# Optimization experiments

Hardware: AMD Instinct MI355X
Metric: run time of the kernel (lower is better)

Reference implementation:

```python
import jax, jax.numpy as jnp
import numpy as np

N = 2000
E = 20000
C = 16
B = 128
N_IN = 200   # first N_IN nodes are input nodes
N_OUT = 200  # last N_OUT nodes are output nodes
EPS = 1e-5


def setup_inputs() -> dict:
    key = jax.random.key(0)
    ks = jax.random.split(key, 8)
    x = jax.random.normal(ks[0], (B, N), dtype=jnp.float32)
    edge_index = jax.random.randint(ks[1], (2, E), 0, N, dtype=jnp.int32)
    input_node_mask = jnp.arange(N) < N_IN
    output_node_mask = jnp.arange(N) >= (N - N_OUT)
    func_mask = ~(input_node_mask | output_node_mask)
    # sparse-linear parameters (structured forms of W1/W2/W3)
    w1 = jax.random.normal(ks[2], (E, C), dtype=jnp.float32) * (1.0 / np.sqrt(C))
    b1 = jnp.zeros((N, C), dtype=jnp.float32)
    w2 = jax.random.normal(ks[3], (N, C, C), dtype=jnp.float32) * (1.0 / np.sqrt(C))
    b2 = jnp.zeros((N, C), dtype=jnp.float32)
    w3 = jax.random.normal(ks[4], (E, C), dtype=jnp.float32) * 1.0  # d=1 init scale
    b3 = jnp.zeros((E,), dtype=jnp.float32)
    g1 = jnp.ones((N * C,), dtype=jnp.float32)
    be1 = jnp.zeros((N * C,), dtype=jnp.float32)
    g2 = jnp.ones((N * C,), dtype=jnp.float32)
    be2 = jnp.zeros((N * C,), dtype=jnp.float32)
    return {"x": x, "w1": w1, "b1": b1, "w2": w2, "b2": b2, "w3": w3, "b3": b3,
            "g1": g1, "be1": be1, "g2": g2, "be2": be2,
            "edge_index": edge_index, "func_mask": func_mask,
            "output_node_mask": output_node_mask, "layers": 4}


def _batchnorm(h, g, b):
    # training-mode BatchNorm1d: batch mean and biased variance over axis 0
    m = h.mean(axis=0)
    v = h.var(axis=0)
    return (h - m) * jax.lax.rsqrt(v + EPS) * g + b


def reference(x, w1, b1, w2, b2, w3, b3, g1, be1, g2, be2,
              edge_index, func_mask, output_node_mask, layers):
    src, dst = edge_index[0], edge_index[1]
    Bsz, Nn = x.shape
    Ee, Cc = w1.shape
    fm = func_mask.astype(x.dtype)
    w2m = w2 * fm[:, None, None]          # W2 blocks exist only at function nodes
    w3m = w3 * fm[src][:, None]           # W3 rows exist only for edges with src in function nodes

    x0 = x[:, src]                        # node2edge: (B, E)
    xe = x0
    for _ in range(layers):
        # lin1: scatter edge values into dst node hidden channels
        contrib = xe.T[:, :, None] * w1[:, None, :]                    # (E, B, C)
        h = jax.ops.segment_sum(contrib, dst, num_segments=Nn)         # (N, B, C)
        h = jnp.transpose(h, (1, 0, 2)) + b1                           # (B, N, C)
        h = _batchnorm(h.reshape(Bsz, Nn * Cc), g1, be1)
        h = jax.nn.elu(h).reshape(Bsz, Nn, Cc)
        # lin2: block-diagonal C x C mix per (function) node
        h = jnp.einsum('bnc,ncd->bnd', h, w2m) + b2
        h = _batchnorm(h.reshape(Bsz, Nn * Cc), g2, be2)
        h = jax.nn.elu(h).reshape(Bsz, Nn, Cc)
        # lin3: gather src hidden, per-edge dot back to edge space
        xe = jnp.einsum('bec,ec->be', h[:, src], w3m) + b3             # (B, E)
        xe = xe + x0
    # edge2node: scatter-sum edge values to dst nodes, keep output nodes
    nodes = jax.ops.segment_sum(xe.T, dst, num_segments=Nn)            # (N, B)
    return nodes.T * output_node_mask.astype(x.dtype)
```

## Files before the change

### kernel.cpp

```cpp
#include <hip/hip_runtime.h>
#include <math.h>

#define BB 128
#define NN 2000
#define EE 20000
#define CC 16
#define FUNC_LO 200
#define FUNC_HI 1800
#define OUT_LO 1800
#define NFUNC 1600
#define EPSV 1e-5f
#define SS 40
#define HP 129

__global__ __launch_bounds__(256) void k_prep(
    const float* __restrict__ x, const int* __restrict__ ei,
    const float* __restrict__ w1, const float* __restrict__ w3,
    const float* __restrict__ b3,
    int* __restrict__ degIn, int* __restrict__ degOut,
    int* __restrict__ posIn,
    float* __restrict__ xT, float* __restrict__ w1s, float* __restrict__ w3s,
    float* __restrict__ b3s, int* __restrict__ inoff, int* __restrict__ wout,
    int* __restrict__ dstn, float* __restrict__ out)
{
    int t = blockIdx.x * 256 + threadIdx.x;
    if (t < EE) {
        int s = ei[t], d = ei[EE + t];
        int p = atomicAdd(&degIn[d], 1);
        int q = atomicAdd(&degOut[s], 1);
        int pi = d * SS + p, po = s * SS + q;
        posIn[t] = pi;
        inoff[pi] = s * BB;
        wout[po]  = pi * BB;
        dstn[po]  = d;
        b3s[po]   = b3[t];
        const float4* w1r = (const float4*)(w1 + (size_t)t * CC);
        float4*       w1d = (float4*)(w1s + (size_t)pi * CC);
        const float4* w3r = (const float4*)(w3 + (size_t)t * CC);
        float4*       w3d = (float4*)(w3s + (size_t)po * CC);
        #pragma unroll
        for (int i = 0; i < 4; i++) { w1d[i] = w1r[i]; w3d[i] = w3r[i]; }
    }
    if (t < NN * BB) {
        int b = t / NN, n = t - b * NN;
        xT[n * BB + b] = x[t];
        out[t] = 0.0f;
    }
}

__global__ __launch_bounds__(128) void k_fill(
    const int* __restrict__ ei, const int* __restrict__ posIn,
    const float* __restrict__ b3, const float* __restrict__ xT,
    float* __restrict__ xeA, float* __restrict__ xeB, float* __restrict__ out)
{
    int e = blockIdx.x;
    int s = ei[e];
    if (s >= FUNC_LO && s < FUNC_HI) return;
    int d = ei[EE + e];
    int b = threadIdx.x;
    float val = b3[e] + xT[s * BB + b];
    if (d >= FUNC_LO && d < FUNC_HI) {
        int ro = posIn[e] * BB;
        xeA[ro + b] = val;
        xeB[ro + b] = val;
    } else if (d >= OUT_LO) {
        atomicAdd(&out[(size_t)b * NN + d], val);
    }
}

__device__ __forceinline__ void bn_elu(float (&t)[CC],
                                       const float* __restrict__ g,
                                       const float* __restrict__ be,
                                       float* tile, float* part_s, float* part_ss,
                                       float* sc, float* sh, int b) {
    #pragma unroll
    for (int c = 0; c < CC; c++) tile[c * HP + b] = t[c];
    __syncthreads();
    {
        int c = b & 15, grp = b >> 4;
        float s = 0.f, ss = 0.f;
        #pragma unroll
        for (int i = 0; i < 16; i++) {
            float v = tile[c * HP + grp * 16 + i];
            s += v; ss += v * v;
        }
        part_s[grp * 16 + c] = s;
        part_ss[grp * 16 + c] = ss;
    }
    __syncthreads();
    if (b < CC) {
        float S = 0.f, SSm = 0.f;
        #pragma unroll
        for (int g8 = 0; g8 < 8; g8++) { S += part_s[g8 * 16 + b]; SSm += part_ss[g8 * 16 + b]; }
        float mean = S * (1.0f / BB);
        float var = SSm * (1.0f / BB) - mean * mean;
        float scale = rsqrtf(var + EPSV) * g[b];
        sc[b] = scale;
        sh[b] = be[b] - mean * scale;
    }
    __syncthreads();
    #pragma unroll
    for (int c = 0; c < CC; c++) {
        float u = t[c] * sc[c] + sh[c];
        t[c] = (u > 0.0f) ? u : (__expf(u) - 1.0f);
    }
}

__global__ __launch_bounds__(128) void k_layer(
    const float* __restrict__ xe_in, const int* __restrict__ inoff,
    const float* __restrict__ xT,
    const float* __restrict__ w1s, const float* __restrict__ w2,
    const float* __restrict__ w3s, const float* __restrict__ b3s,
    const int* __restrict__ wout, const int* __restrict__ dstn,
    const float* __restrict__ g1, const float* __restrict__ be1,
    const float* __restrict__ g2, const float* __restrict__ be2,
    const int* __restrict__ degIn, const int* __restrict__ degOut,
    float* __restrict__ xe_out, float* __restrict__ out, int lastFlag)
{
    const int b = threadIdx.x;
    const int n = FUNC_LO + blockIdx.x;
    const int base = n * SS;

    __shared__ float tile[CC * HP];
    __shared__ float part_s[128], part_ss[128];
    __shared__ float sc[CC], sh[CC];

    int dIn = degIn[n];
    int dOut = degOut[n];
    float x0r = xT[n * BB + b];

    float a[CC];
    #pragma unroll
    for (int c = 0; c < CC; c++) a[c] = 0.0f;

    for (int k0 = 0; k0 < dIn; k0 += 8) {
        float v[8];
        #pragma unroll
        for (int j = 0; j < 8; j++) {
            v[j] = 0.0f;
            if (k0 + j < dIn) {
                int ro = inoff ? inoff[base + k0 + j] : (base + k0 + j) * BB;
                v[j] = xe_in[ro + b];
            }
        }
        #pragma unroll
        for (int j = 0; j < 8; j++) {
            if (k0 + j < dIn) {
                const float* wr = &w1s[(size_t)(base + k0 + j) * CC];
                #pragma unroll
                for (int c = 0; c < CC; c++) a[c] += v[j] * wr[c];
            }
        }
    }

    bn_elu(a, g1 + n * CC, be1 + n * CC, tile, part_s, part_ss, sc, sh, b);

    float h2[CC];
    #pragma unroll
    for (int d = 0; d < CC; d++) h2[d] = 0.0f;
    const float* w2n = w2 + n * (CC * CC);
    #pragma unroll
    for (int c = 0; c < CC; c++) {
        float av = a[c];
        #pragma unroll
        for (int d = 0; d < CC; d++) h2[d] += av * w2n[c * CC + d];
    }

    bn_elu(h2, g2 + n * CC, be2 + n * CC, tile, part_s, part_ss, sc, sh, b);

    for (int q0 = 0; q0 < dOut; q0 += 4) {
        #pragma unroll
        for (int j = 0; j < 4; j++) {
            int q = q0 + j;
            if (q >= dOut) break;
            int sl = base + q;
            int dn = dstn[sl];
            bool live = lastFlag ? (dn >= OUT_LO) : (dn >= FUNC_LO && dn < FUNC_HI);
            if (!live) continue;
            const float* wr = &w3s[(size_t)sl * CC];
            float val = b3s[sl] + x0r;
            #pragma unroll
            for (int d = 0; d < CC; d++) val += h2[d] * wr[d];
            if (lastFlag) atomicAdd(&out[(size_t)b * NN + dn], val);
            else          xe_out[wout[sl] + b] = val;
        }
    }
}

extern "C" void kernel_launch(void* const* d_in, const int* in_sizes, int n_in,
                              void* d_out, int out_size, void* d_ws, size_t ws_size,
                              hipStream_t stream) {
    const float* x   = (const float*)d_in[0];
    const float* w1  = (const float*)d_in[1];
    const float* w2  = (const float*)d_in[3];
    const float* w3  = (const float*)d_in[5];
    const float* b3  = (const float*)d_in[6];
    const float* g1  = (const float*)d_in[7];
    const float* be1 = (const float*)d_in[8];
    const float* g2  = (const float*)d_in[9];
    const float* be2 = (const float*)d_in[10];
    const int* ei    = (const int*)d_in[11];
    float* out = (float*)d_out;

    char* ws = (char*)d_ws;
    float* xT   = (float*)ws;  ws += (size_t)NN * BB * 4;
    float* xeA  = (float*)ws;  ws += (size_t)NN * SS * BB * 4;
    float* xeB  = (float*)ws;  ws += (size_t)NN * SS * BB * 4;
    float* w1s  = (float*)ws;  ws += (size_t)NN * SS * CC * 4;
    float* w3s  = (float*)ws;  ws += (size_t)NN * SS * CC * 4;
    float* b3s  = (float*)ws;  ws += (size_t)NN * SS * 4;
    int* degIn  = (int*)ws;    ws += (size_t)NN * 4;
    int* degOut = (int*)ws;    ws += (size_t)NN * 4;
    int* posIn  = (int*)ws;    ws += (size_t)EE * 4;
    int* inoff  = (int*)ws;    ws += (size_t)NN * SS * 4;
    int* wout   = (int*)ws;    ws += (size_t)NN * SS * 4;
    int* dstn   = (int*)ws;    ws += (size_t)NN * SS * 4;

    hipMemsetAsync(degIn, 0, 2 * NN * sizeof(int), stream);
    k_prep<<<(NN * BB) / 256, 256, 0, stream>>>(x, ei, w1, w3, b3, degIn, degOut,
                                                posIn, xT, w1s, w3s, b3s,
                                                inoff, wout, dstn, out);
    k_fill<<<EE, 128, 0, stream>>>(ei, posIn, b3, xT, xeA, xeB, out);

    const int* nullp = nullptr;
    k_layer<<<NFUNC, 128, 0, stream>>>(xT,  inoff, xT, w1s, w2, w3s, b3s, wout, dstn,
                                       g1, be1, g2, be2, degIn, degOut, xeA, out, 0);
    k_layer<<<NFUNC, 128, 0, stream>>>(xeA, nullp, xT, w1s, w2, w3s, b3s, wout, dstn,
                                       g1, be1, g2, be2, degIn, degOut, xeB, out, 0);
    k_layer<<<NFUNC, 128, 0, stream>>>(xeB, nullp, xT, w1s, w2, w3s, b3s, wout, dstn,
                                       g1, be1, g2, be2, degIn, degOut, xeA, out, 0);
    k_layer<<<NFUNC, 128, 0, stream>>>(xeA, nullp, xT, w1s, w2, w3s, b3s, wout, dstn,
                                       g1, be1, g2, be2, degIn, degOut, xeB, out, 1);
}
```

Measured before the change: 181.6 us.

## Split edge gather/scatter across two thread halves and transpose output accumulation

Doubles the layer kernel block to 256 threads so two halves share the incoming-edge gather and outgoing-edge scatter for a node. The halves combine partial sums through shared memory, and the BN statistics are reduced by 256 threads. Output accumulation moves to a compact transposed buffer so atomics from one wavefront hit contiguous addresses, and a new finalize kernel writes the full output. The cost is extra syncs, redundant lin2 compute in both halves, and one more kernel launch.

After: 194.8 us. 1.07x slower.

```diff
diff --git a/kernel.cpp b/kernel.cpp
--- a/kernel.cpp
+++ b/kernel.cpp
@@ -8,6 +8,7 @@
 #define FUNC_LO 200
 #define FUNC_HI 1800
 #define OUT_LO 1800
+#define OUTN 200
 #define NFUNC 1600
 #define EPSV 1e-5f
 #define SS 40
@@ -21,7 +22,7 @@
     int* __restrict__ posIn,
     float* __restrict__ xT, float* __restrict__ w1s, float* __restrict__ w3s,
     float* __restrict__ b3s, int* __restrict__ inoff, int* __restrict__ wout,
-    int* __restrict__ dstn, float* __restrict__ out)
+    int* __restrict__ dstn, float* __restrict__ outT)
 {
     int t = blockIdx.x * 256 + threadIdx.x;
     if (t < EE) {
@@ -44,14 +45,14 @@
     if (t < NN * BB) {
         int b = t / NN, n = t - b * NN;
         xT[n * BB + b] = x[t];
-        out[t] = 0.0f;
-    }
+    }
+    if (t < OUTN * BB) outT[t] = 0.0f;
 }
 
 __global__ __launch_bounds__(128) void k_fill(
     const int* __restrict__ ei, const int* __restrict__ posIn,
     const float* __restrict__ b3, const float* __restrict__ xT,
-    float* __restrict__ xeA, float* __restrict__ xeB, float* __restrict__ out)
+    float* __restrict__ xeA, float* __restrict__ xeB, float* __restrict__ outT)
 {
     int e = blockIdx.x;
     int s = ei[e];
@@ -64,49 +65,11 @@
         xeA[ro + b] = val;
         xeB[ro + b] = val;
     } else if (d >= OUT_LO) {
-        atomicAdd(&out[(size_t)b * NN + d], val);
-    }
-}
-
-__device__ __forceinline__ void bn_elu(float (&t)[CC],
-                                       const float* __restrict__ g,
-                                       const float* __restrict__ be,
-                                       float* tile, float* part_s, float* part_ss,
-                                       float* sc, float* sh, int b) {
-    #pragma unroll
-    for (int c = 0; c < CC; c++) tile[c * HP + b] = t[c];
-    __syncthreads();
-    {
-        int c = b & 15, grp = b >> 4;
-        float s = 0.f, ss = 0.f;
-        #pragma unroll
-        for (int i = 0; i < 16; i++) {
-            float v = tile[c * HP + grp * 16 + i];
-            s += v; ss += v * v;
-        }
-        part_s[grp * 16 + c] = s;
-        part_ss[grp * 16 + c] = ss;
-    }
-    __syncthreads();
-    if (b < CC) {
-        float S = 0.f, SSm = 0.f;
-        #pragma unroll
-        for (int g8 = 0; g8 < 8; g8++) { S += part_s[g8 * 16 + b]; SSm += part_ss[g8 * 16 + b]; }
-        float mean = S * (1.0f / BB);
-        float var = SSm * (1.0f / BB) - mean * mean;
-        float scale = rsqrtf(var + EPSV) * g[b];
-        sc[b] = scale;
-        sh[b] = be[b] - mean * scale;
-    }
-    __syncthreads();
-    #pragma unroll
-    for (int c = 0; c < CC; c++) {
-        float u = t[c] * sc[c] + sh[c];
-        t[c] = (u > 0.0f) ? u : (__expf(u) - 1.0f);
-    }
-}
-
-__global__ __launch_bounds__(128) void k_layer(
+        atomicAdd(&outT[(d - OUT_LO) * BB + b], val);
+    }
+}
+
+__global__ __launch_bounds__(256) void k_layer(
     const float* __restrict__ xe_in, const int* __restrict__ inoff,
     const float* __restrict__ xT,
     const float* __restrict__ w1s, const float* __restrict__ w2,
@@ -115,15 +78,17 @@
     const float* __restrict__ g1, const float* __restrict__ be1,
     const float* __restrict__ g2, const float* __restrict__ be2,
     const int* __restrict__ degIn, const int* __restrict__ degOut,
-    float* __restrict__ xe_out, float* __restrict__ out, int lastFlag)
+    float* __restrict__ xe_out, float* __restrict__ outT, int lastFlag)
 {
-    const int b = threadIdx.x;
+    const int tid = threadIdx.x;
+    const int b = tid & 127;
+    const int half = tid >> 7;
     const int n = FUNC_LO + blockIdx.x;
     const int base = n * SS;
 
     __shared__ float tile[CC * HP];
-    __shared__ float part_s[128], part_ss[128];
-    __shared__ float sc[CC], sh[CC];
+    __shared__ float part_s[256], part_ss[256];
+    __shared__ float sc[CC], sh[CC], sc2[CC], sh2[CC];
 
     int dIn = degIn[n];
     int dOut = degOut[n];
@@ -133,7 +98,7 @@
     #pragma unroll
     for (int c = 0; c < CC; c++) a[c] = 0.0f;
 
-    for (int k0 = 0; k0 < dIn; k0 += 8) {
+    for (int k0 = half * 8; k0 < dIn; k0 += 16) {
         float v[8];
         #pragma unroll
         for (int j = 0; j < 8; j++) {
@@ -153,7 +118,40 @@
         }
     }
 
-    bn_elu(a, g1 + n * CC, be1 + n * CC, tile, part_s, part_ss, sc, sh, b);
+    if (half == 0) {
+        #pragma unroll
+        for (int c = 0; c < CC; c++) tile[c * HP + b] = a[c];
+    }
+    __syncthreads();
+    if (half == 1) {
+        #pragma unroll
+        for (int c = 0; c < CC; c++) tile[c * HP + b] += a[c];
+    }
+    __syncthreads();
+
+    {
+        int c = tid & 15, grp = tid >> 4;
+        float s = 0.f, ss = 0.f;
+        #pragma unroll
+        for (int i = 0; i < 8; i++) {
+            float v = tile[c * HP + grp * 8 + i];
+            s += v; ss += v * v;
+        }
+        part_s[grp * 16 + c] = s;
+        part_ss[grp * 16 + c] = ss;
+    }
+    __syncthreads();
+    if (tid < CC) {
+        float S = 0.f, SSm = 0.f;
+        #pragma unroll
+        for (int g16 = 0; g16 < 16; g16++) { S += part_s[g16 * 16 + tid]; SSm += part_ss[g16 * 16 + tid]; }
+        float mean = S * (1.0f / BB);
+        float var = SSm * (1.0f / BB) - mean * mean;
+        float scale = rsqrtf(var + EPSV) * g1[n * CC + tid];
+        sc[tid] = scale;
+        sh[tid] = be1[n * CC + tid] - mean * scale;
+    }
+    __syncthreads();
 
     float h2[CC];
     #pragma unroll
@@ -161,29 +159,68 @@
     const float* w2n = w2 + n * (CC * CC);
     #pragma unroll
     for (int c = 0; c < CC; c++) {
-        float av = a[c];
+        float u = tile[c * HP + b] * sc[c] + sh[c];
+        float av = (u > 0.0f) ? u : (__expf(u) - 1.0f);
         #pragma unroll
         for (int d = 0; d < CC; d++) h2[d] += av * w2n[c * CC + d];
     }
-
-    bn_elu(h2, g2 + n * CC, be2 + n * CC, tile, part_s, part_ss, sc, sh, b);
-
-    for (int q0 = 0; q0 < dOut; q0 += 4) {
-        #pragma unroll
-        for (int j = 0; j < 4; j++) {
-            int q = q0 + j;
-            if (q >= dOut) break;
-            int sl = base + q;
-            int dn = dstn[sl];
-            bool live = lastFlag ? (dn >= OUT_LO) : (dn >= FUNC_LO && dn < FUNC_HI);
-            if (!live) continue;
-            const float* wr = &w3s[(size_t)sl * CC];
-            float val = b3s[sl] + x0r;
-            #pragma unroll
-            for (int d = 0; d < CC; d++) val += h2[d] * wr[d];
-            if (lastFlag) atomicAdd(&out[(size_t)b * NN + dn], val);
-            else          xe_out[wout[sl] + b] = val;
-        }
+    __syncthreads();
+
+    if (half == 0) {
+        #pragma unroll
+        for (int c = 0; c < CC; c++) tile[c * HP + b] = h2[c];
+    }
+    __syncthreads();
+    {
+        int c = tid & 15, grp = tid >> 4;
+        float s = 0.f, ss = 0.f;
+        #pragma unroll
+        for (int i = 0; i < 8; i++) {
+            float v = tile[c * HP + grp * 8 + i];
+            s += v; ss += v * v;
+        }
+        part_s[grp * 16 + c] = s;
+        part_ss[grp * 16 + c] = ss;
+    }
+    __syncthreads();
+    if (tid < CC) {
+        float S = 0.f, SSm = 0.f;
+        #pragma unroll
+        for (int g16 = 0; g16 < 16; g16++) { S += part_s[g16 * 16 + tid]; SSm += part_ss[g16 * 16 + tid]; }
+        float mean = S * (1.0f / BB);
+        float var = SSm * (1.0f / BB) - mean * mean;
+        float scale = rsqrtf(var + EPSV) * g2[n * CC + tid];
+        sc2[tid] = scale;
+        sh2[tid] = be2[n * CC + tid] - mean * scale;
+    }
+    __syncthreads();
+
+    #pragma unroll
+    for (int c = 0; c < CC; c++) {
+        float u = h2[c] * sc2[c] + sh2[c];
+        h2[c] = (u > 0.0f) ? u : (__expf(u) - 1.0f);
+    }
+
+    for (int q = half; q < dOut; q += 2) {
+        int sl = base + q;
+        int dn = dstn[sl];
+        bool live = lastFlag ? (dn >= OUT_LO) : (dn >= FUNC_LO && dn < FUNC_HI);
+        if (!live) continue;
+        const float* wr = &w3s[(size_t)sl * CC];
+        float val = b3s[sl] + x0r;
+        #pragma unroll
+        for (int d = 0; d < CC; d++) val += h2[d] * wr[d];
+        if (lastFlag) atomicAdd(&outT[(dn - OUT_LO) * BB + b], val);
+        else          xe_out[wout[sl] + b] = val;
+    }
+}
+
+__global__ void k_finalize(const float* __restrict__ outT, float* __restrict__ out) {
+    int idx = blockIdx.x * 256 + threadIdx.x;
+    if (idx < BB * NN) {
+        int b = idx / NN;
+        int n = idx - b * NN;
+        out[idx] = (n >= OUT_LO) ? outT[(n - OUT_LO) * BB + b] : 0.0f;
     }
 }
 
@@ -209,6 +246,7 @@
     float* w1s  = (float*)ws;  ws += (size_t)NN * SS * CC * 4;
     float* w3s  = (float*)ws;  ws += (size_t)NN * SS * CC * 4;
     float* b3s  = (float*)ws;  ws += (size_t)NN * SS * 4;
+    float* outT = (float*)ws;  ws += (size_t)OUTN * BB * 4;
     int* degIn  = (int*)ws;    ws += (size_t)NN * 4;
     int* degOut = (int*)ws;    ws += (size_t)NN * 4;
     int* posIn  = (int*)ws;    ws += (size_t)EE * 4;
@@ -219,16 +257,18 @@
     hipMemsetAsync(degIn, 0, 2 * NN * sizeof(int), stream);
     k_prep<<<(NN * BB) / 256, 256, 0, stream>>>(x, ei, w1, w3, b3, degIn, degOut,
                                                 posIn, xT, w1s, w3s, b3s,
-                                                inoff, wout, dstn, out);
-    k_fill<<<EE, 128, 0, stream>>>(ei, posIn, b3, xT, xeA, xeB, out);
+                                                inoff, wout, dstn, outT);
+    k_fill<<<EE, 128, 0, stream>>>(ei, posIn, b3, xT, xeA, xeB, outT);
 
     const int* nullp = nullptr;
-    k_layer<<<NFUNC, 128, 0, stream>>>(xT,  inoff, xT, w1s, w2, w3s, b3s, wout, dstn,
-                                       g1, be1, g2, be2, degIn, degOut, xeA, out, 0);
-    k_layer<<<NFUNC, 128, 0, stream>>>(xeA, nullp, xT, w1s, w2, w3s, b3s, wout, dstn,
-                                       g1, be1, g2, be2, degIn, degOut, xeB, out, 0);
-    k_layer<<<NFUNC, 128, 0, stream>>>(xeB, nullp, xT, w1s, w2, w3s, b3s, wout, dstn,
-                                       g1, be1, g2, be2, degIn, degOut, xeA, out, 0);
-    k_layer<<<NFUNC, 128, 0, stream>>>(xeA, nullp, xT, w1s, w2, w3s, b3s, wout, dstn,
-                                       g1, be1, g2, be2, degIn, degOut, xeB, out, 1);
-}
+    k_layer<<<NFUNC, 256, 0, stream>>>(xT,  inoff, xT, w1s, w2, w3s, b3s, wout, dstn,
+                                       g1, be1, g2, be2, degIn, degOut, xeA, outT, 0);
+    k_layer<<<NFUNC, 256, 0, stream>>>(xeA, nullp, xT, w1s, w2, w3s, b3s, wout, dstn,
+                                       g1, be1, g2, be2, degIn, degOut, xeB, outT, 0);
+    k_layer<<<NFUNC, 256, 0, stream>>>(xeB, nullp, xT, w1s, w2, w3s, b3s, wout, dstn,
+                                       g1, be1, g2, be2, degIn, degOut, xeA, outT, 0);
+    k_layer<<<NFUNC, 256, 0, stream>>>(xeA, nullp, xT, w1s, w2, w3s, b3s, wout, dstn,
+                                       g1, be1, g2, be2, degIn, degOut, xeB, outT, 1);
+
+    k_finalize<<<(NN * BB + 255) / 256, 256, 0, stream>>>(outT, out);
+}
```
